# Kernel tuning notes

Hardware: AMD Instinct MI355X
Metric: run time of the kernel (lower is better)

Reference implementation:

```python
import jax, jax.numpy as jnp
import numpy as np

B, RATIO, IN_CH, H = 32, 32, 64, 8
E = IN_CH * H                 # embed_dim = in_channels * n_heads = 512
NODES_PER_GRAPH = 512
N = B * NODES_PER_GRAPH       # 16384 source nodes


def setup_inputs() -> dict:
    key = jax.random.key(0)
    ks = jax.random.split(key, 6)
    x = jax.random.normal(ks[0], (N, E), dtype=jnp.float32)
    # edge_index is accepted by forward but unused in 'attn' mode
    edge_index = jax.random.randint(ks[1], (2, 262144), 0, N, dtype=jnp.int32)
    # per-node graph id, sorted, equal-size graphs (batch[-1] + 1 == B)
    batch = jnp.repeat(jnp.arange(B, dtype=jnp.int32), NODES_PER_GRAPH)
    # learned params: cluster query seeds + MultiheadAttention in/out projections
    xcent_base = jax.random.normal(ks[2], (RATIO, E), dtype=jnp.float32)
    in_proj_w = jax.random.normal(ks[3], (3 * E, E), dtype=jnp.float32) / np.sqrt(E).astype(np.float32)
    in_proj_b = jnp.zeros((3 * E,), dtype=jnp.float32)
    out_proj_w = jax.random.normal(ks[4], (E, E), dtype=jnp.float32) / np.sqrt(E).astype(np.float32)
    out_proj_b = jnp.zeros((E,), dtype=jnp.float32)
    return dict(x=x, edge_index=edge_index, batch=batch, xcent_base=xcent_base,
                in_proj_w=in_proj_w, in_proj_b=in_proj_b,
                out_proj_w=out_proj_w, out_proj_b=out_proj_b)


def reference(x, edge_index, batch, xcent_base, in_proj_w, in_proj_b, out_proj_w, out_proj_b):
    # BipartPool.forward, mode='attn':
    #   x_aggrs = xcent_base.repeat(batch_size, 1)  -> queries [L, E], L = B*ratio
    #   MultiheadAttention(q=x_aggrs, k=v=x, attn_mask=mask[batch].T)
    # mask[batch].T is True (disallowed) where query's graph != node's graph.
    L = B * RATIO
    head_dim = E // H
    x_aggrs = jnp.tile(xcent_base, (B, 1))                        # [L, E]

    wq, wk, wv = jnp.split(in_proj_w, 3, axis=0)                  # each [E, E]
    bq, bk, bv = jnp.split(in_proj_b, 3, axis=0)
    q = (x_aggrs @ wq.T + bq).reshape(L, H, head_dim).transpose(1, 0, 2)  # [H, L, hd]
    k = (x @ wk.T + bk).reshape(N, H, head_dim).transpose(1, 0, 2)        # [H, N, hd]
    v = (x @ wv.T + bv).reshape(N, H, head_dim).transpose(1, 0, 2)        # [H, N, hd]

    batchcent = jnp.repeat(jnp.arange(B, dtype=batch.dtype), RATIO)       # [L]
    allowed = batchcent[:, None] == batch[None, :]                        # [L, N]

    scale = np.float32(1.0 / np.sqrt(head_dim))
    scores = jnp.einsum('hld,hnd->hln', q, k) * scale                     # [H, L, N]
    scores = jnp.where(allowed[None], scores, -jnp.inf)
    attn = jax.nn.softmax(scores, axis=-1)
    out = jnp.einsum('hln,hnd->hld', attn, v)                             # [H, L, hd]
    out = out.transpose(1, 0, 2).reshape(L, E)
    xcent = out @ out_proj_w.T + out_proj_b                               # [L, E]
    # original returns (xcent.reshape(B, ratio, E), None, None, batchcent, None, None)
    return xcent.reshape(B, RATIO, E), batchcent
```

## Files before the change

### kernel.cpp

```cpp
#include <hip/hip_runtime.h>
#include <hip/hip_bf16.h>

#define NGRAPH 32
#define NHEAD 8
#define EMB 512
#define NNODES 16384
#define NPG 512
#define LQ 1024
#define PST 520
#define GCH 262144

typedef __attribute__((ext_vector_type(8))) short short8;
typedef __attribute__((ext_vector_type(4))) float f32x4;

static __device__ __forceinline__ unsigned short f2bf(float f) {
  union { float f; unsigned u; } v; v.f = f;
  unsigned r = (v.u + 0x7fffu + ((v.u >> 16) & 1u)) >> 16;
  return (unsigned short)r;
}

static __device__ __forceinline__ short8 cvt8(float4 a, float4 b) {
  short8 r;
  r[0] = f2bf(a.x); r[1] = f2bf(a.y); r[2] = f2bf(a.z); r[3] = f2bf(a.w);
  r[4] = f2bf(b.x); r[5] = f2bf(b.y); r[6] = f2bf(b.z); r[7] = f2bf(b.w);
  return r;
}

static __device__ __forceinline__ void gload_lds16(const ushort* g, ushort* l) {
  __builtin_amdgcn_global_load_lds(
      (const __attribute__((address_space(1))) unsigned*)g,
      (__attribute__((address_space(3))) unsigned*)l, 16, 0, 0);
}

#define BARRIER_LGKM()                                        \
  do {                                                        \
    asm volatile("s_waitcnt lgkmcnt(0)" ::: "memory");        \
    __builtin_amdgcn_s_barrier();                             \
  } while (0)

__global__ __launch_bounds__(256) void prep_all(
    const float* __restrict__ x, const float* __restrict__ wv,
    const float* __restrict__ wo, const float* __restrict__ wq,
    const float* __restrict__ wk, const float* __restrict__ xc,
    const float* __restrict__ bq,
    ushort* __restrict__ xbC, ushort* __restrict__ xbTC,
    ushort* __restrict__ wvb, ushort* __restrict__ wob,
    ushort* __restrict__ PCb, float* __restrict__ bcent) {
  __shared__ ushort smemU[11776];
  const int b = blockIdx.x;
  const int t = threadIdx.x;

  if (b < 2048) {
    ushort* tile = smemU;
    int xr = b & 7, j = b >> 3;
    int m = j >> 6, r = j & 63;
    int g = xr + 8 * m;
    int bc = r & 7;
    int bl = r >> 3;
    int n0 = bl * 64, e0 = bc * 64;
    int trr = t >> 4, tc = t & 15;
#pragma unroll
    for (int p = 0; p < 4; ++p) {
      int n = trr + p * 16;
      long gi = (long)(g * NPG + n0 + n) * EMB + e0 + tc * 4;
      float4 v = *reinterpret_cast<const float4*>(x + gi);
      ushort4 o;
      o.x = f2bf(v.x); o.y = f2bf(v.y); o.z = f2bf(v.z); o.w = f2bf(v.w);
      *reinterpret_cast<ushort4*>(&tile[n * 72 + tc * 4]) = o;
    }
    __syncthreads();
    {
      int n = t >> 2, pp = t & 3;
      int ng = n0 + n;
      int sp = pp ^ ((ng >> 1) & 3);
#pragma unroll
      for (int kcq = 0; kcq < 2; ++kcq) {
        int kc = bc * 2 + kcq;
        short8 v = *reinterpret_cast<const short8*>(&tile[n * 72 + kcq * 32 + sp * 8]);
        *reinterpret_cast<short8*>(
            &xbC[(long)g * GCH + kc * 16384 + ng * 32 + pp * 8]) = v;
      }
      int e = t >> 2;
      int eg = e0 + e;
      int sp2 = (t & 3) ^ ((eg >> 1) & 3);
#pragma unroll
      for (int ncq = 0; ncq < 2; ++ncq) {
        int nc = bl * 2 + ncq;
        ushort tmp[8];
#pragma unroll
        for (int jj = 0; jj < 8; ++jj)
          tmp[jj] = tile[(ncq * 32 + sp2 * 8 + jj) * 72 + e];
        *reinterpret_cast<short8*>(
            &xbTC[(long)g * GCH + nc * 16384 + eg * 32 + (t & 3) * 8]) =
            *reinterpret_cast<short8*>(tmp);
      }
    }
    return;
  }

  if (b < 2560) {
    int off = b - 2048;
    const float* src = (off < 256) ? wv : wo;
    ushort* dst = (off < 256) ? wvb : wob;
    off &= 255;
    int i = (off * 256 + t) * 4;
    float4 v = *reinterpret_cast<const float4*>(src + i);
    ushort4 o;
    o.x = f2bf(v.x); o.y = f2bf(v.y); o.z = f2bf(v.z); o.w = f2bf(v.w);
    *reinterpret_cast<ushort4*>(dst + i) = o;
    return;
  }

  if (b == 2560) {
#pragma unroll
    for (int p = 0; p < 4; ++p) bcent[t + p * 256] = (float)((t + p * 256) >> 5);
    return;
  }

  {
    ushort* Qs  = smemU;
    ushort* WkT = smemU + 2304;
    int qb = b - 2561;
    int h = qb >> 2, qs = qb & 3;
    int w = t >> 6, lane = t & 63;
    int lr = lane & 15, grp = lane >> 4, ko = grp * 8;

    {
      int dl = t >> 2, cq = t & 3;
      const float* wr = wk + (long)(h * 64 + dl) * EMB + qs * 128;
#pragma unroll
      for (int m = 0; m < 8; ++m) {
        int c0 = cq * 32 + m * 4;
        float4 v = *reinterpret_cast<const float4*>(wr + c0);
        WkT[(c0 + 0) * 72 + dl] = f2bf(0.125f * v.x);
        WkT[(c0 + 1) * 72 + dl] = f2bf(0.125f * v.y);
        WkT[(c0 + 2) * 72 + dl] = f2bf(0.125f * v.z);
        WkT[(c0 + 3) * 72 + dl] = f2bf(0.125f * v.w);
      }
    }

    f32x4 qa[2];
    qa[0] = (f32x4)(0.0f); qa[1] = (f32x4)(0.0f);
#pragma unroll 4
    for (int kk = 0; kk < EMB; kk += 32) {
      const float* xr0 = xc + lr * EMB + kk + ko;
      const float* xr1 = xc + (16 + lr) * EMB + kk + ko;
      const float* wr  = wq + (long)(h * 64 + w * 16 + lr) * EMB + kk + ko;
      short8 a0 = cvt8(*reinterpret_cast<const float4*>(xr0),
                       *reinterpret_cast<const float4*>(xr0 + 4));
      short8 a1 = cvt8(*reinterpret_cast<const float4*>(xr1),
                       *reinterpret_cast<const float4*>(xr1 + 4));
      short8 bb = cvt8(*reinterpret_cast<const float4*>(wr),
                       *reinterpret_cast<const float4*>(wr + 4));
      qa[0] = __builtin_amdgcn_mfma_f32_16x16x32_bf16(a0, bb, qa[0], 0, 0, 0);
      qa[1] = __builtin_amdgcn_mfma_f32_16x16x32_bf16(a1, bb, qa[1], 0, 0, 0);
    }
    float bias = bq[h * 64 + w * 16 + lr];
#pragma unroll
    for (int i = 0; i < 2; ++i)
#pragma unroll
      for (int r = 0; r < 4; ++r)
        Qs[(i * 16 + grp * 4 + r) * 72 + w * 16 + lr] = f2bf(qa[i][r] + bias);
    __syncthreads();

    f32x4 pa[2][2];
#pragma unroll
    for (int i = 0; i < 2; ++i)
#pragma unroll
      for (int j = 0; j < 2; ++j) pa[i][j] = (f32x4)(0.0f);
#pragma unroll
    for (int kk = 0; kk < 64; kk += 32) {
      short8 a0 = *reinterpret_cast<const short8*>(&Qs[lr * 72 + kk + ko]);
      short8 a1 = *reinterpret_cast<const short8*>(&Qs[(16 + lr) * 72 + kk + ko]);
#pragma unroll
      for (int j = 0; j < 2; ++j) {
        short8 bb = *reinterpret_cast<const short8*>(
            &WkT[(w * 32 + j * 16 + lr) * 72 + kk + ko]);
        pa[0][j] = __builtin_amdgcn_mfma_f32_16x16x32_bf16(a0, bb, pa[0][j], 0, 0, 0);
        pa[1][j] = __builtin_amdgcn_mfma_f32_16x16x32_bf16(a1, bb, pa[1][j], 0, 0, 0);
      }
    }
#pragma unroll
    for (int i = 0; i < 2; ++i)
#pragma unroll
      for (int j = 0; j < 2; ++j)
#pragma unroll
        for (int r = 0; r < 4; ++r)
          PCb[(long)(h * 32 + i * 16 + grp * 4 + r) * EMB + qs * 128 + w * 32 + j * 16 + lr] =
              f2bf(pa[i][j][r]);
  }
}

__global__ __launch_bounds__(1024) void fused_attn(
    const ushort* __restrict__ PCb, const ushort* __restrict__ xbC,
    const ushort* __restrict__ xbTC, const ushort* __restrict__ wvb,
    const float* __restrict__ bvb, ushort* __restrict__ aout) {
  __shared__ ushort PCl[32 * PST];
  __shared__ ushort PBuf[32 * PST];
  __shared__ ushort Bbuf[2][16384];
  __shared__ float rmax[32][16];
  __shared__ float rsum[32][16];

  const int g = blockIdx.x & 31, h = blockIdx.x >> 5;
  const int t = threadIdx.x, w = t >> 6, lane = t & 63;
  const int lr = lane & 15, grp = lane >> 4;
  const int koU = grp * 8;

  const ushort* xgC  = xbC  + (long)g * GCH;
  const ushort* xgTC = xbTC + (long)g * GCH;

  auto STAGE1 = [&](int c, int db) {
#pragma unroll
    for (int q = 0; q < 2; ++q)
      gload_lds16(xgC + c * 16384 + (w * 32 + q * 16) * 32 + lane * 8,
                  &Bbuf[db][(w * 32 + q * 16) * 32]);
  };
  auto STAGE3 = [&](int c, int db) {
#pragma unroll
    for (int q = 0; q < 2; ++q)
      gload_lds16(xgTC + c * 16384 + (w * 32 + q * 16) * 32 + lane * 8,
                  &Bbuf[db][(w * 32 + q * 16) * 32]);
  };

  STAGE1(0, 0);
  STAGE1(1, 1);
  {
    const ushort* pc = PCb + h * 32 * EMB;
#pragma unroll
    for (int p = 0; p < 2; ++p) {
      int u = t + p * 1024;
      int row = u >> 6, col = (u & 63) * 8;
      *reinterpret_cast<short8*>(&PCl[row * PST + col]) =
          *reinterpret_cast<const short8*>(pc + row * EMB + col);
    }
  }
  BARRIER_LGKM();

  f32x4 acc[2][2];
#pragma unroll
  for (int i = 0; i < 2; ++i)
#pragma unroll
    for (int j = 0; j < 2; ++j) acc[i][j] = (f32x4)(0.0f);

#pragma unroll
  for (int c = 0; c < 16; ++c) {
    const int db = c & 1;
    asm volatile("s_waitcnt vmcnt(2)" ::: "memory");
    __builtin_amdgcn_sched_barrier(0);
    short8 a0 = *reinterpret_cast<const short8*>(&PCl[lr * PST + c * 32 + koU]);
    short8 a1 = *reinterpret_cast<const short8*>(&PCl[(16 + lr) * PST + c * 32 + koU]);
    short8 bv8[2];
#pragma unroll
    for (int j = 0; j < 2; ++j) {
      int n = w * 32 + j * 16 + lr;
      int psrc = grp ^ ((n >> 1) & 3);
      bv8[j] = *reinterpret_cast<const short8*>(&Bbuf[db][n * 32 + psrc * 8]);
    }
#pragma unroll
    for (int j = 0; j < 2; ++j) {
      acc[0][j] = __builtin_amdgcn_mfma_f32_16x16x32_bf16(a0, bv8[j], acc[0][j], 0, 0, 0);
      acc[1][j] = __builtin_amdgcn_mfma_f32_16x16x32_bf16(a1, bv8[j], acc[1][j], 0, 0, 0);
    }
    __builtin_amdgcn_sched_barrier(0);
    if (c < 14) STAGE1(c + 2, db);
    else        STAGE3(c - 14, db);
  }

#pragma unroll
  for (int i = 0; i < 2; ++i)
#pragma unroll
    for (int r = 0; r < 4; ++r) {
      float m = fmaxf(acc[i][0][r], acc[i][1][r]);
      m = fmaxf(m, __shfl_xor(m, 1)); m = fmaxf(m, __shfl_xor(m, 2));
      m = fmaxf(m, __shfl_xor(m, 4)); m = fmaxf(m, __shfl_xor(m, 8));
      if (lr == 0) rmax[i * 16 + grp * 4 + r][w] = m;
    }
  BARRIER_LGKM();
#pragma unroll
  for (int i = 0; i < 2; ++i)
#pragma unroll
    for (int r = 0; r < 4; ++r) {
      int row = i * 16 + grp * 4 + r;
      float m = rmax[row][0];
#pragma unroll
      for (int q = 1; q < 16; ++q) m = fmaxf(m, rmax[row][q]);
      float s = 0.f;
#pragma unroll
      for (int j = 0; j < 2; ++j) {
        float e = __expf(acc[i][j][r] - m);
        acc[i][j][r] = e;
        s += e;
      }
      s += __shfl_xor(s, 1); s += __shfl_xor(s, 2);
      s += __shfl_xor(s, 4); s += __shfl_xor(s, 8);
      if (lr == 0) rsum[row][w] = s;
    }
  BARRIER_LGKM();
#pragma unroll
  for (int i = 0; i < 2; ++i)
#pragma unroll
    for (int r = 0; r < 4; ++r) {
      int row = i * 16 + grp * 4 + r;
      float tot = rsum[row][0];
#pragma unroll
      for (int q = 1; q < 16; ++q) tot += rsum[row][q];
      float inv = 1.f / tot;
#pragma unroll
      for (int j = 0; j < 2; ++j)
        PBuf[row * PST + w * 32 + j * 16 + lr] = f2bf(acc[i][j][r] * inv);
    }
  BARRIER_LGKM();

  f32x4 acc2[2][2];
#pragma unroll
  for (int i = 0; i < 2; ++i)
#pragma unroll
    for (int j = 0; j < 2; ++j) acc2[i][j] = (f32x4)(0.0f);

#pragma unroll
  for (int c = 0; c < 16; ++c) {
    const int db = c & 1;
    if (c < 15) asm volatile("s_waitcnt vmcnt(2)" ::: "memory");
    else        asm volatile("s_waitcnt vmcnt(0)" ::: "memory");
    __builtin_amdgcn_sched_barrier(0);
    short8 a0 = *reinterpret_cast<const short8*>(&PBuf[lr * PST + c * 32 + koU]);
    short8 a1 = *reinterpret_cast<const short8*>(&PBuf[(16 + lr) * PST + c * 32 + koU]);
    short8 bv8[2];
#pragma unroll
    for (int j = 0; j < 2; ++j) {
      int e = w * 32 + j * 16 + lr;
      int psrc = grp ^ ((e >> 1) & 3);
      bv8[j] = *reinterpret_cast<const short8*>(&Bbuf[db][e * 32 + psrc * 8]);
    }
#pragma unroll
    for (int j = 0; j < 2; ++j) {
      acc2[0][j] = __builtin_amdgcn_mfma_f32_16x16x32_bf16(a0, bv8[j], acc2[0][j], 0, 0, 0);
      acc2[1][j] = __builtin_amdgcn_mfma_f32_16x16x32_bf16(a1, bv8[j], acc2[1][j], 0, 0, 0);
    }
    __builtin_amdgcn_sched_barrier(0);
    if (c < 14) STAGE3(c + 2, db);
  }
  BARRIER_LGKM();

#pragma unroll
  for (int i = 0; i < 2; ++i)
#pragma unroll
    for (int r = 0; r < 4; ++r) {
      int row = i * 16 + grp * 4 + r;
#pragma unroll
      for (int j = 0; j < 2; ++j)
        PBuf[row * PST + w * 32 + j * 16 + lr] = f2bf(acc2[i][j][r]);
    }
  BARRIER_LGKM();

  if (w < 8) {
    int wr = w >> 2, wc = w & 3;
    f32x4 acc3 = (f32x4)(0.0f);
    const ushort* wvh = wvb + (long)(h * 64 + wc * 16) * EMB;
#pragma unroll
    for (int c = 0; c < 16; ++c) {
      short8 a = *reinterpret_cast<const short8*>(&PBuf[(wr * 16 + lr) * PST + c * 32 + koU]);
      short8 b = *reinterpret_cast<const short8*>(wvh + (long)lr * EMB + c * 32 + koU);
      acc3 = __builtin_amdgcn_mfma_f32_16x16x32_bf16(a, b, acc3, 0, 0, 0);
    }
    float bias = bvb[h * 64 + wc * 16 + lr];
#pragma unroll
    for (int r = 0; r < 4; ++r) {
      int row = wr * 16 + grp * 4 + r;
      aout[(long)(g * 32 + row) * EMB + h * 64 + wc * 16 + lr] = f2bf(acc3[r] + bias);
    }
  }
}

template <int KK, int FM, int FN, int WM, int WN, bool OUT_BF16, bool HAS_BIAS>
__global__ void gemm_abt(const ushort* __restrict__ A, const ushort* __restrict__ Bm,
                         void* __restrict__ C, const float* __restrict__ bias,
                         int lda, int ldb, int ldc) {
  int tid = threadIdx.x;
  int wave = tid >> 6, lane = tid & 63;
  int wr = wave / WN, wc = wave % WN;
  int rowBase = blockIdx.y * (WM * FM * 16) + wr * FM * 16;
  int colBase = blockIdx.x * (WN * FN * 16) + wc * FN * 16;
  int lr = lane & 15;
  int ko = (lane >> 4) * 8;

  f32x4 acc[FM][FN];
#pragma unroll
  for (int i = 0; i < FM; ++i)
#pragma unroll
    for (int j = 0; j < FN; ++j) acc[i][j] = (f32x4)(0.0f);

#pragma unroll 8
  for (int kk = 0; kk < KK; kk += 32) {
    short8 av[FM], bv[FN];
#pragma unroll
    for (int i = 0; i < FM; ++i)
      av[i] = *reinterpret_cast<const short8*>(A + (long)(rowBase + i * 16 + lr) * lda + kk + ko);
#pragma unroll
    for (int j = 0; j < FN; ++j)
      bv[j] = *reinterpret_cast<const short8*>(Bm + (long)(colBase + j * 16 + lr) * ldb + kk + ko);
#pragma unroll
    for (int i = 0; i < FM; ++i)
#pragma unroll
      for (int j = 0; j < FN; ++j)
        acc[i][j] = __builtin_amdgcn_mfma_f32_16x16x32_bf16(av[i], bv[j], acc[i][j], 0, 0, 0);
  }

  int or0 = (lane >> 4) * 4;
#pragma unroll
  for (int i = 0; i < FM; ++i) {
#pragma unroll
    for (int j = 0; j < FN; ++j) {
      int col = colBase + j * 16 + lr;
      float bval = HAS_BIAS ? bias[col] : 0.f;
#pragma unroll
      for (int r = 0; r < 4; ++r) {
        int row = rowBase + i * 16 + or0 + r;
        float v = acc[i][j][r] + bval;
        if (OUT_BF16)
          ((ushort*)C)[(long)row * ldc + col] = f2bf(v);
        else
          ((float*)C)[(long)row * ldc + col] = v;
      }
    }
  }
}

extern "C" void kernel_launch(void* const* d_in, const int* in_sizes, int n_in,
                              void* d_out, int out_size, void* d_ws, size_t ws_size,
                              hipStream_t stream) {
  const float* x          = (const float*)d_in[0];
  const float* xcent_base = (const float*)d_in[3];
  const float* in_proj_w  = (const float*)d_in[4];
  const float* in_proj_b  = (const float*)d_in[5];
  const float* out_proj_w = (const float*)d_in[6];
  const float* out_proj_b = (const float*)d_in[7];

  char* w = (char*)d_ws;
  ushort* xbC  = (ushort*)(w);
  ushort* xbTC = (ushort*)(w + 16777216);
  ushort* PCb  = (ushort*)(w + 33554432);
  ushort* wvb  = (ushort*)(w + 33816576);
  ushort* wob  = (ushort*)(w + 34340864);
  ushort* aout = (ushort*)(w + 34865152);

  const float* wq = in_proj_w;
  const float* wk = in_proj_w + 512 * 512;
  const float* wv = in_proj_w + 1024 * 512;
  const float* bq = in_proj_b;
  const float* bv = in_proj_b + 1024;

  prep_all<<<2593, 256, 0, stream>>>(x, wv, out_proj_w, wq, wk, xcent_base, bq,
                                     xbC, xbTC, wvb, wob, PCb,
                                     (float*)d_out + (long)LQ * EMB);

  fused_attn<<<256, 1024, 0, stream>>>(PCb, xbC, xbTC, wvb, bv, aout);

  gemm_abt<512, 1, 2, 2, 2, false, true><<<dim3(8, 32, 1), 256, 0, stream>>>(
      aout, wob, d_out, out_proj_b, 512, 512, 512);
}
```

Measured before the change: 65.60 us.

## Restructure x conversion blocks with prefetching and reorder prep block roles

The prep kernel's x-to-bf16 conversion now gives each block 128 nodes instead of 64, halving the block count. Each block prefetches the next 32-row chunk of x into registers while the current chunk is written to the row-major bf16 layout. The transposed copy is staged through fp32 shared memory and converted when read out. The small Q·Wk projection blocks move to the front of the grid so their longer work starts first. The per-chunk barriers add synchronization, and the fp32 staging doubles shared-memory traffic for the transpose.

```diff
diff --git a/kernel.cpp b/kernel.cpp
--- a/kernel.cpp
+++ b/kernel.cpp
@@ -46,82 +46,14 @@
     ushort* __restrict__ xbC, ushort* __restrict__ xbTC,
     ushort* __restrict__ wvb, ushort* __restrict__ wob,
     ushort* __restrict__ PCb, float* __restrict__ bcent) {
-  __shared__ ushort smemU[11776];
+  __shared__ __align__(16) ushort smemU[11776];
   const int b = blockIdx.x;
   const int t = threadIdx.x;
 
-  if (b < 2048) {
-    ushort* tile = smemU;
-    int xr = b & 7, j = b >> 3;
-    int m = j >> 6, r = j & 63;
-    int g = xr + 8 * m;
-    int bc = r & 7;
-    int bl = r >> 3;
-    int n0 = bl * 64, e0 = bc * 64;
-    int trr = t >> 4, tc = t & 15;
-#pragma unroll
-    for (int p = 0; p < 4; ++p) {
-      int n = trr + p * 16;
-      long gi = (long)(g * NPG + n0 + n) * EMB + e0 + tc * 4;
-      float4 v = *reinterpret_cast<const float4*>(x + gi);
-      ushort4 o;
-      o.x = f2bf(v.x); o.y = f2bf(v.y); o.z = f2bf(v.z); o.w = f2bf(v.w);
-      *reinterpret_cast<ushort4*>(&tile[n * 72 + tc * 4]) = o;
-    }
-    __syncthreads();
-    {
-      int n = t >> 2, pp = t & 3;
-      int ng = n0 + n;
-      int sp = pp ^ ((ng >> 1) & 3);
-#pragma unroll
-      for (int kcq = 0; kcq < 2; ++kcq) {
-        int kc = bc * 2 + kcq;
-        short8 v = *reinterpret_cast<const short8*>(&tile[n * 72 + kcq * 32 + sp * 8]);
-        *reinterpret_cast<short8*>(
-            &xbC[(long)g * GCH + kc * 16384 + ng * 32 + pp * 8]) = v;
-      }
-      int e = t >> 2;
-      int eg = e0 + e;
-      int sp2 = (t & 3) ^ ((eg >> 1) & 3);
-#pragma unroll
-      for (int ncq = 0; ncq < 2; ++ncq) {
-        int nc = bl * 2 + ncq;
-        ushort tmp[8];
-#pragma unroll
-        for (int jj = 0; jj < 8; ++jj)
-          tmp[jj] = tile[(ncq * 32 + sp2 * 8 + jj) * 72 + e];
-        *reinterpret_cast<short8*>(
-            &xbTC[(long)g * GCH + nc * 16384 + eg * 32 + (t & 3) * 8]) =
-            *reinterpret_cast<short8*>(tmp);
-      }
-    }
-    return;
-  }
-
-  if (b < 2560) {
-    int off = b - 2048;
-    const float* src = (off < 256) ? wv : wo;
-    ushort* dst = (off < 256) ? wvb : wob;
-    off &= 255;
-    int i = (off * 256 + t) * 4;
-    float4 v = *reinterpret_cast<const float4*>(src + i);
-    ushort4 o;
-    o.x = f2bf(v.x); o.y = f2bf(v.y); o.z = f2bf(v.z); o.w = f2bf(v.w);
-    *reinterpret_cast<ushort4*>(dst + i) = o;
-    return;
-  }
-
-  if (b == 2560) {
-#pragma unroll
-    for (int p = 0; p < 4; ++p) bcent[t + p * 256] = (float)((t + p * 256) >> 5);
-    return;
-  }
-
-  {
+  if (b < 32) {
     ushort* Qs  = smemU;
     ushort* WkT = smemU + 2304;
-    int qb = b - 2561;
-    int h = qb >> 2, qs = qb & 3;
+    int h = b >> 2, qs = b & 3;
     int w = t >> 6, lane = t & 63;
     int lr = lane & 15, grp = lane >> 4, ko = grp * 8;
 
@@ -188,7 +120,77 @@
         for (int r = 0; r < 4; ++r)
           PCb[(long)(h * 32 + i * 16 + grp * 4 + r) * EMB + qs * 128 + w * 32 + j * 16 + lr] =
               f2bf(pa[i][j][r]);
-  }
+    return;
+  }
+
+  if (b < 1056) {
+    float* tf = (float*)smemU;
+    int local = b - 32;
+    int xr = local & 7, j = local >> 3;
+    int m = j >> 5, r2 = j & 31;
+    int g = xr + 8 * m;
+    int bc = r2 & 7;
+    int bl = r2 >> 3;
+    int n0 = bl * 128, e0 = bc * 64;
+
+    int nl = t >> 3, e8 = t & 7;
+    int ps = e8 & 3, kc = bc * 2 + (e8 >> 2);
+    int eL = t >> 2, pm2 = t & 3;
+    int eg = e0 + eL;
+    int ps2 = pm2 ^ ((eg >> 1) & 3);
+
+    float4 va[2], vb[2];
+    {
+      const float* p = x + (long)(g * NPG + n0 + nl) * EMB + e0 + e8 * 8;
+      va[0] = *reinterpret_cast<const float4*>(p);
+      vb[0] = *reinterpret_cast<const float4*>(p + 4);
+    }
+#pragma unroll
+    for (int r = 0; r < 4; ++r) {
+      const int cur = r & 1, nxt = cur ^ 1;
+      if (r < 3) {
+        const float* p = x + (long)(g * NPG + n0 + (r + 1) * 32 + nl) * EMB + e0 + e8 * 8;
+        va[nxt] = *reinterpret_cast<const float4*>(p);
+        vb[nxt] = *reinterpret_cast<const float4*>(p + 4);
+      }
+      int ng = n0 + r * 32 + nl;
+      int pm = ps ^ ((ng >> 1) & 3);
+      short8 s8 = cvt8(va[cur], vb[cur]);
+      *reinterpret_cast<short8*>(
+          &xbC[(long)g * GCH + kc * 16384 + ng * 32 + pm * 8]) = s8;
+      *reinterpret_cast<float4*>(&tf[nl * 68 + e8 * 8]) = va[cur];
+      *reinterpret_cast<float4*>(&tf[nl * 68 + e8 * 8 + 4]) = vb[cur];
+      __syncthreads();
+      {
+        int nc = bl * 4 + r;
+        ushort tmp[8];
+#pragma unroll
+        for (int k2 = 0; k2 < 8; ++k2)
+          tmp[k2] = f2bf(tf[(ps2 * 8 + k2) * 68 + eL]);
+        *reinterpret_cast<short8*>(
+            &xbTC[(long)g * GCH + nc * 16384 + eg * 32 + pm2 * 8]) =
+            *reinterpret_cast<short8*>(tmp);
+      }
+      if (r < 3) __syncthreads();
+    }
+    return;
+  }
+
+  if (b < 1568) {
+    int off = b - 1056;
+    const float* src = (off < 256) ? wv : wo;
+    ushort* dst = (off < 256) ? wvb : wob;
+    off &= 255;
+    int i = (off * 256 + t) * 4;
+    float4 v = *reinterpret_cast<const float4*>(src + i);
+    ushort4 o;
+    o.x = f2bf(v.x); o.y = f2bf(v.y); o.z = f2bf(v.z); o.w = f2bf(v.w);
+    *reinterpret_cast<ushort4*>(dst + i) = o;
+    return;
+  }
+
+#pragma unroll
+  for (int p = 0; p < 4; ++p) bcent[t + p * 256] = (float)((t + p * 256) >> 5);
 }
 
 __global__ __launch_bounds__(1024) void fused_attn(
@@ -450,7 +452,7 @@
   const float* bq = in_proj_b;
   const float* bv = in_proj_b + 1024;
 
-  prep_all<<<2593, 256, 0, stream>>>(x, wv, out_proj_w, wq, wk, xcent_base, bq,
+  prep_all<<<1569, 256, 0, stream>>>(x, wv, out_proj_w, wq, wk, xcent_base, bq,
                                      xbC, xbTC, wvb, wob, PCb,
                                      (float*)d_out + (long)LQ * EMB);
 
```

Result: faster. 63.09 us (-3.8%).
